# Performance work log

Measured on AMD Instinct MI355X. Metric: run time of the kernel, lower is better.

Reference implementation:

```python
import jax, jax.numpy as jnp
import numpy as np

TEMPERATURE = 0.07
DELTA = 0.3
KA = 2.0
R = 3
B = 4096
D = 512
K = 4096
N = 131072
N_DICT_KEYS = 3  # len(cluster_result) dict: inst2cluster/centroids/density


def _l2norm(x):
    # torch F.normalize: x / max(||x||, 1e-12)
    return x / jnp.maximum(jnp.linalg.norm(x, axis=-1, keepdims=True), 1e-12)


def _inst_inst(anchor, pos):
    # CE with label 0 on [diag, off-diag] == logsumexp(full row) - diag
    a = _l2norm(anchor)
    p = _l2norm(pos)
    logits = (a @ p.T) / TEMPERATURE  # [B, B]
    return jax.nn.logsumexp(logits, axis=1) - jnp.diagonal(logits)


def _off_diag_idx(b):
    # row i -> column indices [0..b-1] excluding i (row-major boolean-mask order)
    j = jnp.arange(b - 1)[None, :]
    return j + (j >= jnp.arange(b)[:, None]).astype(jnp.int32)


def _inst_proto(anchor, i2c, centroids, density, index):
    b = anchor.shape[0]
    a = _l2norm(anchor)
    oidx = _off_diag_idx(b)
    loss = jnp.zeros(b, dtype=anchor.dtype)
    for r in range(R):
        protos = _l2norm(centroids[r])           # [K, D]
        pid = i2c[r][index]                       # [B]
        sim = a @ protos[pid].T                   # [B, B]
        diag = jnp.diagonal(sim)
        off = jnp.take_along_axis(sim, oidx, axis=1)  # [B, B-1]
        # faithful to original: divide concatenated logits column-wise by density[pid]
        logits = jnp.concatenate([diag[:, None], off], axis=1) / density[r][pid][None, :]
        loss = loss + (jax.nn.logsumexp(logits, axis=1) - logits[:, 0])
        loss = loss / N_DICT_KEYS  # original divides INSIDE the loop
    return loss


def _weights(audio, frame, a_i2c, a_cent, f_i2c, f_cent, index):
    fa = _l2norm(audio)
    ff = _l2norm(frame)
    rho = jnp.sum(fa * ff, axis=1)  # diagonal of fa @ ff.T
    for r in range(R):
        ca = a_cent[r][a_i2c[r][index]]  # [B, D] (NOT normalized, as in original)
        cf = f_cent[r][f_i2c[r][index]]
        rho = rho - jnp.sum(ca * cf, axis=1)  # diagonal of ca @ cf.T
    order = jnp.argsort(rho)
    sorted_rho = rho[order]
    mu = rho.mean() + DELTA * rho.std()
    sigma = rho.std() * jnp.sqrt(jnp.asarray(KA, rho.dtype))
    y = jnp.exp(-0.5 * ((sorted_rho - mu) / sigma) ** 2) / (jnp.sqrt(2.0 * jnp.pi) * sigma)
    y = jnp.cumsum(y)
    y = y / y[-1]
    w = y[jnp.argsort(order)]  # y at the rank of each rho_i
    return jax.lax.stop_gradient(w)  # original detaches via cpu().numpy()


def _forward(audio_emb, frame_emb, a_centroids, a_density, f_centroids, f_density,
             video_index, a_inst2cluster, f_inst2cluster):
    loss_v2f_ii = _inst_inst(audio_emb, frame_emb)
    loss_f2v_ii = _inst_inst(frame_emb, audio_emb)
    loss_v2f_ip = _inst_proto(audio_emb, f_inst2cluster, f_centroids, f_density, video_index)
    loss_f2v_ip = _inst_proto(frame_emb, a_inst2cluster, a_centroids, a_density, video_index)
    w = _weights(audio_emb, frame_emb, a_inst2cluster, a_centroids,
                 f_inst2cluster, f_centroids, video_index)
    loss_v2f = jnp.sum(w * (loss_v2f_ii + loss_v2f_ip)) / jnp.sum(w)
    loss_f2v = jnp.sum(w * (loss_f2v_ii + loss_f2v_ip)) / jnp.sum(w)
    return loss_v2f + loss_f2v


def setup_inputs() -> dict:
    key = jax.random.key(0)
    ks = jax.random.split(key, 9)
    return {
        "audio_emb": jax.random.normal(ks[0], (B, D), jnp.float32),
        "frame_emb": jax.random.normal(ks[1], (B, D), jnp.float32),
        "a_centroids": jax.random.normal(ks[2], (R, K, D), jnp.float32),
        "a_density": jax.random.uniform(ks[3], (R, K), jnp.float32, 0.3, 1.3),
        "f_centroids": jax.random.normal(ks[4], (R, K, D), jnp.float32),
        "f_density": jax.random.uniform(ks[5], (R, K), jnp.float32, 0.3, 1.3),
        "video_index": jax.random.randint(ks[6], (B,), 0, N),
        "a_inst2cluster": jax.random.randint(ks[7], (R, N), 0, K),
        "f_inst2cluster": jax.random.randint(ks[8], (R, N), 0, K),
    }


def reference(audio_emb, frame_emb, a_centroids, a_density, f_centroids, f_density,
              video_index, a_inst2cluster, f_inst2cluster):
    return _forward(audio_emb, frame_emb, a_centroids, a_density, f_centroids, f_density,
                    video_index, a_inst2cluster, f_inst2cluster)
```

## Files before the change

### kernel.cpp

```cpp
#include <hip/hip_runtime.h>
#include <math.h>

#define B 4096
#define D 512
#define KC 4096
#define NIDX 131072
#define RR 3
#define TEMP 0.07f
#define M_II 14.5f
#define M_IP 4.0f

typedef __bf16 bf16x8 __attribute__((ext_vector_type(8)));
typedef float f32x4 __attribute__((ext_vector_type(4)));

__device__ __forceinline__ void gload_lds16(const void* g, void* l) {
  __builtin_amdgcn_global_load_lds(
      (const __attribute__((address_space(1))) unsigned int*)g,
      (__attribute__((address_space(3))) unsigned int*)l, 16, 0, 0);
}

__device__ __forceinline__ float dot8(float4 a0, float4 a1, float4 b0, float4 b1) {
  return a0.x * b0.x + a0.y * b0.y + a0.z * b0.z + a0.w * b0.w
       + a1.x * b1.x + a1.y * b1.y + a1.z * b1.z + a1.w * b1.w;
}

__global__ __launch_bounds__(256) void prep_kernel(
    const float* __restrict__ audio, const float* __restrict__ frame,
    const float* __restrict__ a_cent, const float* __restrict__ a_dens,
    const float* __restrict__ f_cent, const float* __restrict__ f_dens,
    const int* __restrict__ vidx, const int* __restrict__ a_i2c,
    const int* __restrict__ f_i2c,
    __bf16* __restrict__ Xa, __bf16* __restrict__ Xf,
    __bf16* __restrict__ Yf, __bf16* __restrict__ Ya,
    float* __restrict__ invdd_f, float* __restrict__ invdd_a,
    float* __restrict__ rho0, float* __restrict__ pcp) {
  const int u = blockIdx.x * 4 + (threadIdx.x >> 6);
  const int lane = threadIdx.x & 63;

  if (u < 2 * B) {
    const float* src; __bf16* dst;
    if (u < B) { src = audio + (size_t)u * D; dst = Xa + (size_t)u * D; }
    else       { src = frame + (size_t)(u - B) * D; dst = Xf + (size_t)(u - B) * D; }
    const float4* s4 = (const float4*)src + lane * 2;
    float4 v0 = s4[0], v1 = s4[1];
    float ss = dot8(v0, v1, v0, v1);
    #pragma unroll
    for (int off = 32; off >= 1; off >>= 1) ss += __shfl_xor(ss, off, 64);
    float invn = 1.f / fmaxf(sqrtf(ss), 1e-12f);
    __bf16 o[8];
    o[0] = (__bf16)(v0.x * invn); o[1] = (__bf16)(v0.y * invn);
    o[2] = (__bf16)(v0.z * invn); o[3] = (__bf16)(v0.w * invn);
    o[4] = (__bf16)(v1.x * invn); o[5] = (__bf16)(v1.y * invn);
    o[6] = (__bf16)(v1.z * invn); o[7] = (__bf16)(v1.w * invn);
    *(bf16x8*)(dst + lane * 8) = *(bf16x8*)o;
  } else if (u < 5 * B) {
    const int q = u - 2 * B;
    const int r = q >> 12;
    const int j = q & (B - 1);
    const int idx = vidx[j];
    const int fp = f_i2c[r * NIDX + idx];
    const int ap = a_i2c[r * NIDX + idx];
    const float4* fr4 = (const float4*)(f_cent + ((size_t)r * KC + fp) * D) + lane * 2;
    const float4* ar4 = (const float4*)(a_cent + ((size_t)r * KC + ap) * D) + lane * 2;
    float4 f0 = fr4[0], f1 = fr4[1];
    float4 a0 = ar4[0], a1 = ar4[1];
    float sf = dot8(f0, f1, f0, f1);
    float sa = dot8(a0, a1, a0, a1);
    float pc = dot8(a0, a1, f0, f1);
    #pragma unroll
    for (int off = 32; off >= 1; off >>= 1) {
      sf += __shfl_xor(sf, off, 64);
      sa += __shfl_xor(sa, off, 64);
      pc += __shfl_xor(pc, off, 64);
    }
    float invnf = 1.f / fmaxf(sqrtf(sf), 1e-12f);
    float invna = 1.f / fmaxf(sqrtf(sa), 1e-12f);
    const int slot = r * B + j;
    __bf16 of[8], oa[8];
    of[0] = (__bf16)(f0.x * invnf); of[1] = (__bf16)(f0.y * invnf);
    of[2] = (__bf16)(f0.z * invnf); of[3] = (__bf16)(f0.w * invnf);
    of[4] = (__bf16)(f1.x * invnf); of[5] = (__bf16)(f1.y * invnf);
    of[6] = (__bf16)(f1.z * invnf); of[7] = (__bf16)(f1.w * invnf);
    oa[0] = (__bf16)(a0.x * invna); oa[1] = (__bf16)(a0.y * invna);
    oa[2] = (__bf16)(a0.z * invna); oa[3] = (__bf16)(a0.w * invna);
    oa[4] = (__bf16)(a1.x * invna); oa[5] = (__bf16)(a1.y * invna);
    oa[6] = (__bf16)(a1.z * invna); oa[7] = (__bf16)(a1.w * invna);
    *(bf16x8*)(Yf + (size_t)slot * D + lane * 8) = *(bf16x8*)of;
    *(bf16x8*)(Ya + (size_t)slot * D + lane * 8) = *(bf16x8*)oa;
    if (lane == 0) {
      invdd_f[slot] = 1.f / f_dens[(size_t)r * KC + fp];
      invdd_a[slot] = 1.f / a_dens[(size_t)r * KC + ap];
      pcp[slot] = pc;
    }
  } else {
    const int i = u - 5 * B;
    const float4* x4 = (const float4*)(audio + (size_t)i * D) + lane * 2;
    const float4* y4 = (const float4*)(frame + (size_t)i * D) + lane * 2;
    float4 a0 = x4[0], a1 = x4[1], f0 = y4[0], f1 = y4[1];
    float saf = dot8(a0, a1, f0, f1);
    float sa = dot8(a0, a1, a0, a1);
    float sf = dot8(f0, f1, f0, f1);
    #pragma unroll
    for (int off = 32; off >= 1; off >>= 1) {
      saf += __shfl_xor(saf, off, 64);
      sa  += __shfl_xor(sa, off, 64);
      sf  += __shfl_xor(sf, off, 64);
    }
    if (lane == 0)
      rho0[i] = saf / (fmaxf(sqrtf(sa), 1e-12f) * fmaxf(sqrtf(sf), 1e-12f));
  }
}

__global__ __launch_bounds__(256) void lse_mfma_kernel(
    const __bf16* __restrict__ Xa, const __bf16* __restrict__ Xf,
    const __bf16* __restrict__ Yf, const __bf16* __restrict__ Ya,
    const float* __restrict__ invdd_f, const float* __restrict__ invdd_a,
    float* __restrict__ sp, float* __restrict__ colsp,
    float* __restrict__ diagAll) {
  __shared__ __bf16 As[128 * 32];
  __shared__ __bf16 Bs[128 * 32];
  __shared__ float inv_lds[2][132];
  __shared__ float part_s[2 * 128];
  __shared__ float colpart[2][128];

  const int yy = blockIdx.y;
  const int job = (yy == 0) ? 0 : yy + 1;
  const int hf = blockIdx.z;
  const int i0 = blockIdx.x * 128;

  const __bf16* Ab; const __bf16* Bb; const float* invArr = nullptr;
  if (job == 0)      { Ab = Xa; Bb = Xf; }
  else if (job <= 4) { Ab = Xa; Bb = Yf + (size_t)(job - 2) * B * D;
                       invArr = invdd_f + (job - 2) * B; }
  else               { Ab = Xf; Bb = Ya + (size_t)(job - 5) * B * D;
                       invArr = invdd_a + (job - 5) * B; }
  const bool ii = (job == 0);
  const float invT = 1.f / TEMP;
  const float inv0 = ii ? invT : invArr[0];
  const float MJ = ii ? M_II : M_IP;

  const int tid = threadIdx.x;
  const int wv = tid >> 6;
  const int lane = tid & 63;
  const int wr = (wv >> 1) * 64;
  const int wc = (wv & 1) * 64;
  const int g = lane >> 4;
  const int cl = lane & 15;

  const int srow = lane >> 2;
  const int skoff = (((lane & 3) ^ ((lane >> 3) & 3)) * 16);
  const int c0row = wv * 16 + srow;
  const int c1row = 64 + wv * 16 + srow;
  const char* gA0 = (const char*)Ab + (size_t)(i0 + c0row) * (D * 2) + skoff;
  const char* gA1 = (const char*)Ab + (size_t)(i0 + c1row) * (D * 2) + skoff;
  __bf16* lA0 = As + wv * 512;
  __bf16* lA1 = As + 2048 + wv * 512;
  __bf16* lB0 = Bs + wv * 512;
  __bf16* lB1 = Bs + 2048 + wv * 512;

  const int csw = (g ^ ((cl >> 1) & 3)) * 8;
  int aoff[4], boff[4];
  #pragma unroll
  for (int t = 0; t < 4; ++t) {
    aoff[t] = (wr + t * 16 + cl) * 32 + csw;
    boff[t] = (wc + t * 16 + cl) * 32 + csw;
  }

  float sacc[4][4];
  #pragma unroll
  for (int ri = 0; ri < 4; ++ri)
    #pragma unroll
    for (int v = 0; v < 4; ++v) sacc[ri][v] = 0.f;

  for (int jt = hf * 4; jt < hf * 4 + 4; ++jt) {
    const int j0 = jt * 128;
    float* invL = inv_lds[jt & 1];
    if (!ii && tid < 130) {
      int idx = j0 + tid; if (idx > B - 1) idx = B - 1;
      invL[tid] = invArr[idx];
    }
    const char* gB0 = (const char*)Bb + (size_t)(j0 + c0row) * (D * 2) + skoff;
    const char* gB1 = (const char*)Bb + (size_t)(j0 + c1row) * (D * 2) + skoff;

    f32x4 acc[4][4];
    #pragma unroll
    for (int ri = 0; ri < 4; ++ri)
      #pragma unroll
      for (int ci = 0; ci < 4; ++ci) acc[ri][ci] = (f32x4){0.f, 0.f, 0.f, 0.f};

    for (int kt = 0; kt < 16; ++kt) {
      __syncthreads();
      const int kb = kt * 64;
      gload_lds16(gA0 + kb, lA0);
      gload_lds16(gA1 + kb, lA1);
      gload_lds16(gB0 + kb, lB0);
      gload_lds16(gB1 + kb, lB1);
      __syncthreads();
      bf16x8 af[4], bfr[4];
      #pragma unroll
      for (int t = 0; t < 4; ++t) {
        af[t] = *(const bf16x8*)(As + aoff[t]);
        bfr[t] = *(const bf16x8*)(Bs + boff[t]);
      }
      #pragma unroll
      for (int ri = 0; ri < 4; ++ri)
        #pragma unroll
        for (int ci = 0; ci < 4; ++ci)
          acc[ri][ci] = __builtin_amdgcn_mfma_f32_16x16x32_bf16(
              af[ri], bfr[ci], acc[ri][ci], 0, 0, 0);
    }

    float csum[4] = {0.f, 0.f, 0.f, 0.f};
    #pragma unroll
    for (int ri = 0; ri < 4; ++ri) {
      #pragma unroll
      for (int v = 0; v < 4; ++v) {
        const int gi = i0 + wr + ri * 16 + g * 4 + v;
        float acc4 = 0.f;
        #pragma unroll
        for (int ci = 0; ci < 4; ++ci) {
          const int jloc = wc + ci * 16 + cl;
          const int gj = j0 + jloc;
          float sc;
          if (ii) sc = invT;
          else    sc = (gj == gi) ? inv0 : invL[(gj < gi) ? (jloc + 1) : jloc];
          float lv = acc[ri][ci][v] * sc;
          if (gj == gi) diagAll[(size_t)job * B + gi] = lv;
          float ev = __expf(lv - MJ);
          acc4 += ev;
          if (ii) csum[ci] += ev;
        }
        sacc[ri][v] += acc4;
      }
    }
    if (ii) {
      #pragma unroll
      for (int ci = 0; ci < 4; ++ci) {
        csum[ci] += __shfl_xor(csum[ci], 16, 64);
        csum[ci] += __shfl_xor(csum[ci], 32, 64);
      }
      if (g == 0) {
        #pragma unroll
        for (int ci = 0; ci < 4; ++ci)
          colpart[wv >> 1][wc + ci * 16 + cl] = csum[ci];
      }
      __syncthreads();
      if (tid < 128)
        colsp[(size_t)blockIdx.x * B + j0 + tid] =
            colpart[0][tid] + colpart[1][tid];
    }
  }

  #pragma unroll
  for (int ri = 0; ri < 4; ++ri) {
    #pragma unroll
    for (int v = 0; v < 4; ++v) {
      float s = sacc[ri][v];
      #pragma unroll
      for (int off = 8; off >= 1; off >>= 1) s += __shfl_xor(s, off, 64);
      if (cl == 0) part_s[(wv & 1) * 128 + wr + ri * 16 + g * 4 + v] = s;
    }
  }
  __syncthreads();
  if (tid < 128) {
    size_t o = ((size_t)job * 8 + hf) * B + i0 + tid;
    sp[o] = part_s[tid] + part_s[128 + tid];
  }
}

__global__ __launch_bounds__(256) void merge_rank_kernel(
    const float* __restrict__ sp, const float* __restrict__ colsp,
    const float* __restrict__ diagAll, const float* __restrict__ rho0,
    const float* __restrict__ pcp,
    float* __restrict__ lossAll, int* __restrict__ rankArr,
    float* __restrict__ srho) {
  __shared__ float lr[B];
  __shared__ float cnt[256];
  const int blk = blockIdx.x;
  const int t = threadIdx.x;
  if (blk < 128) {
    int idx = blk * 256 + t;
    int job = idx >> 12;
    int i = idx & (B - 1);
    if (job == 1) {
      float stot = 0.f;
      #pragma unroll 8
      for (int x = 0; x < 32; ++x) stot += colsp[(size_t)x * B + i];
      lossAll[idx] = M_II + logf(stot) - diagAll[i];
    } else {
      const float* s8 = sp + (size_t)job * 8 * B + i;
      float stot = 0.f;
      #pragma unroll
      for (int x = 0; x < 8; ++x) stot += s8[(size_t)x * B];
      float MJ = (job < 2) ? M_II : M_IP;
      lossAll[idx] = MJ + logf(stot) - diagAll[(size_t)job * B + i];
    }
  } else {
    const int base = (blk - 128) * 32;
    const int il = t & 31;
    const int i = base + il;
    const int jlo = (t >> 5) * 512;
    for (int k = t; k < B; k += 256)
      lr[k] = rho0[k] - pcp[k] - pcp[B + k] - pcp[2 * B + k];
    __syncthreads();
    float my = lr[i];
    int rk = 0;
    #pragma unroll 8
    for (int j = jlo; j < jlo + 512; ++j) {
      float v = lr[j];
      rk += (v < my) || (v == my && j < i);
    }
    cnt[t] = (float)rk;
    __syncthreads();
    if (t < 32) {
      int r = 0;
      #pragma unroll
      for (int s = 0; s < 8; ++s) r += (int)cnt[s * 32 + t];
      rankArr[i] = r;
      srho[r] = my;
    }
  }
}

__global__ __launch_bounds__(1024) void cdf_final_kernel(
    const float* __restrict__ srho, const int* __restrict__ rankArr,
    const float* __restrict__ lossAll, float* __restrict__ out) {
  __shared__ float pdf[B];
  __shared__ float wred[16], wr1[16], wr2[16];
  __shared__ float wexc[16];
  __shared__ float mv[3];
  const int t = threadIdx.x;
  const int lane = t & 63;
  const int wid = t >> 6;

  float4 sv = *reinterpret_cast<const float4*>(srho + (size_t)t * 4);
  float s = sv.x + sv.y + sv.z + sv.w;
  #pragma unroll
  for (int off = 32; off >= 1; off >>= 1) s += __shfl_xor(s, off, 64);
  if (lane == 0) wred[wid] = s;
  __syncthreads();
  if (t == 0) {
    float tot = 0.f;
    #pragma unroll
    for (int w = 0; w < 16; ++w) tot += wred[w];
    mv[0] = tot / (float)B;
  }
  __syncthreads();
  const float mean = mv[0];
  __syncthreads();
  float dx = sv.x - mean, dy = sv.y - mean, dz = sv.z - mean, dw = sv.w - mean;
  float v = dx * dx + dy * dy + dz * dz + dw * dw;
  #pragma unroll
  for (int off = 32; off >= 1; off >>= 1) v += __shfl_xor(v, off, 64);
  if (lane == 0) wred[wid] = v;
  __syncthreads();
  if (t == 0) {
    float tot = 0.f;
    #pragma unroll
    for (int w = 0; w < 16; ++w) tot += wred[w];
    float sd = sqrtf(tot / (float)B);
    mv[0] = mean + 0.3f * sd;
    mv[1] = sd * 1.41421356237f;
  }
  __syncthreads();
  const float mu = mv[0], sg = mv[1];
  const float c = 1.f / (2.5066282746310002f * sg);
  float p[4];
  {
    float z0 = (sv.x - mu) / sg; p[0] = expf(-0.5f * z0 * z0) * c;
    float z1 = (sv.y - mu) / sg; p[1] = expf(-0.5f * z1 * z1) * c;
    float z2 = (sv.z - mu) / sg; p[2] = expf(-0.5f * z2 * z2) * c;
    float z3 = (sv.w - mu) / sg; p[3] = expf(-0.5f * z3 * z3) * c;
  }
  float chunk = p[0] + p[1] + p[2] + p[3];
  float incl = chunk;
  #pragma unroll
  for (int d = 1; d < 64; d <<= 1) {
    float n = __shfl_up(incl, d, 64);
    if (lane >= d) incl += n;
  }
  if (lane == 63) wred[wid] = incl;
  __syncthreads();
  if (t == 0) {
    float run = 0.f;
    #pragma unroll
    for (int w = 0; w < 16; ++w) { wexc[w] = run; run += wred[w]; }
    mv[2] = run;
  }
  __syncthreads();
  float run = wexc[wid] + (incl - chunk);
  #pragma unroll
  for (int e = 0; e < 4; ++e) { run += p[e]; pdf[t * 4 + e] = run; }
  const float ylast = mv[2];
  __syncthreads();
  int4 rks = *reinterpret_cast<const int4*>(rankArr + (size_t)t * 4);
  float sw = 0.f, s1 = 0.f, s2 = 0.f;
  #pragma unroll
  for (int e = 0; e < 4; ++e) {
    const int i = t * 4 + e;
    const int rk = (e == 0) ? rks.x : (e == 1) ? rks.y : (e == 2) ? rks.z : rks.w;
    float wi = pdf[rk] / ylast;
    float lpv = lossAll[2 * B + i] * (1.f / 27.f) + lossAll[3 * B + i] * (1.f / 9.f)
              + lossAll[4 * B + i] * (1.f / 3.f);
    float lpf = lossAll[5 * B + i] * (1.f / 27.f) + lossAll[6 * B + i] * (1.f / 9.f)
              + lossAll[7 * B + i] * (1.f / 3.f);
    sw += wi;
    s1 += wi * (lossAll[i] + lpv);
    s2 += wi * (lossAll[B + i] + lpf);
  }
  #pragma unroll
  for (int off = 32; off >= 1; off >>= 1) {
    sw += __shfl_xor(sw, off, 64);
    s1 += __shfl_xor(s1, off, 64);
    s2 += __shfl_xor(s2, off, 64);
  }
  if (lane == 0) { wred[wid] = sw; wr1[wid] = s1; wr2[wid] = s2; }
  __syncthreads();
  if (t == 0) {
    float tw = 0.f, t1 = 0.f, t2 = 0.f;
    #pragma unroll
    for (int w = 0; w < 16; ++w) { tw += wred[w]; t1 += wr1[w]; t2 += wr2[w]; }
    out[0] = t1 / tw + t2 / tw;
  }
}

extern "C" void kernel_launch(void* const* d_in, const int* in_sizes, int n_in,
                              void* d_out, int out_size, void* d_ws, size_t ws_size,
                              hipStream_t stream) {
  const float* audio  = (const float*)d_in[0];
  const float* frame  = (const float*)d_in[1];
  const float* a_cent = (const float*)d_in[2];
  const float* a_dens = (const float*)d_in[3];
  const float* f_cent = (const float*)d_in[4];
  const float* f_dens = (const float*)d_in[5];
  const int* vidx  = (const int*)d_in[6];
  const int* a_i2c = (const int*)d_in[7];
  const int* f_i2c = (const int*)d_in[8];
  float* out = (float*)d_out;

  const size_t BD = (size_t)B * D;
  char* base = (char*)d_ws;
  __bf16* Xa = (__bf16*)base;              base += BD * 2;
  __bf16* Xf = (__bf16*)base;              base += BD * 2;
  __bf16* Yf = (__bf16*)base;              base += 3 * BD * 2;
  __bf16* Ya = (__bf16*)base;              base += 3 * BD * 2;
  float* invdd_f = (float*)base;           base += 3 * B * 4;
  float* invdd_a = (float*)base;           base += 3 * B * 4;
  float* rho0    = (float*)base;           base += B * 4;
  float* pcp     = (float*)base;           base += 3 * B * 4;
  float* sp      = (float*)base;           base += 64 * B * 4;
  float* colsp   = (float*)base;           base += 32 * B * 4;
  float* diagAll = (float*)base;           base += 8 * B * 4;
  float* lossAll = (float*)base;           base += 8 * B * 4;
  float* srho    = (float*)base;           base += B * 4;
  int*   rankArr = (int*)base;

  prep_kernel<<<(6 * B) / 4, 256, 0, stream>>>(audio, frame, a_cent, a_dens,
                                               f_cent, f_dens, vidx, a_i2c, f_i2c,
                                               Xa, Xf, Yf, Ya, invdd_f, invdd_a,
                                               rho0, pcp);

  dim3 g2(B / 128, 7, 8);
  lse_mfma_kernel<<<g2, 256, 0, stream>>>(Xa, Xf, Yf, Ya, invdd_f, invdd_a,
                                          sp, colsp, diagAll);

  merge_rank_kernel<<<256, 256, 0, stream>>>(sp, colsp, diagAll, rho0, pcp,
                                             lossAll, rankArr, srho);
  cdf_final_kernel<<<1, 1024, 0, stream>>>(srho, rankArr, lossAll, out);
}
```

Baseline: 345.5 us.

## Enlarge LSE GEMM tile to 256x256 with 512 threads, one tile per block

The fused similarity/logsumexp MFMA kernel now computes one 256x256 output tile per 512-thread block, where before each 256-thread block looped over four 128x128 column tiles. Each wave holds an 8x4 grid of 16x16 accumulators, so each staged k-slice is reused across more MFMAs. The per-column density scale lookup is simplified to a fixed offset on off-diagonal tiles. This is meant to cut global/LDS traffic per FLOP and per-tile loop overhead. In exchange it raises register pressure (128 accumulator floats per lane plus sacc), which may reduce occupancy, and it doubles the partial-sum buffer read by the merge kernel.

New measurement: 348.2 us. Within noise of the previous version (+0.8%).

```diff
diff --git a/kernel.cpp b/kernel.cpp
--- a/kernel.cpp
+++ b/kernel.cpp
@@ -111,22 +111,22 @@
   }
 }
 
-__global__ __launch_bounds__(256) void lse_mfma_kernel(
+__global__ __launch_bounds__(512) void lse_mfma_kernel(
     const __bf16* __restrict__ Xa, const __bf16* __restrict__ Xf,
     const __bf16* __restrict__ Yf, const __bf16* __restrict__ Ya,
     const float* __restrict__ invdd_f, const float* __restrict__ invdd_a,
     float* __restrict__ sp, float* __restrict__ colsp,
     float* __restrict__ diagAll) {
-  __shared__ __bf16 As[128 * 32];
-  __shared__ __bf16 Bs[128 * 32];
-  __shared__ float inv_lds[2][132];
-  __shared__ float part_s[2 * 128];
-  __shared__ float colpart[2][128];
+  __shared__ __bf16 As[256 * 32];
+  __shared__ __bf16 Bs[256 * 32];
+  __shared__ float invL[260];
+  __shared__ float part_s[4 * 256];
+  __shared__ float colpart[2][256];
 
   const int yy = blockIdx.y;
   const int job = (yy == 0) ? 0 : yy + 1;
-  const int hf = blockIdx.z;
-  const int i0 = blockIdx.x * 128;
+  const int i0 = blockIdx.x * 256;
+  const int j0 = blockIdx.z * 256;
 
   const __bf16* Ab; const __bf16* Bb; const float* invArr = nullptr;
   if (job == 0)      { Ab = Xa; Bb = Xf; }
@@ -142,129 +142,120 @@
   const int tid = threadIdx.x;
   const int wv = tid >> 6;
   const int lane = tid & 63;
-  const int wr = (wv >> 1) * 64;
-  const int wc = (wv & 1) * 64;
+  const int wr = (wv >> 2) * 128;
+  const int wc = (wv & 3) * 64;
   const int g = lane >> 4;
   const int cl = lane & 15;
+
+  if (!ii && tid < 258) {
+    int idx = j0 + tid; if (idx > B - 1) idx = B - 1;
+    invL[tid] = invArr[idx];
+  }
 
   const int srow = lane >> 2;
   const int skoff = (((lane & 3) ^ ((lane >> 3) & 3)) * 16);
   const int c0row = wv * 16 + srow;
-  const int c1row = 64 + wv * 16 + srow;
   const char* gA0 = (const char*)Ab + (size_t)(i0 + c0row) * (D * 2) + skoff;
-  const char* gA1 = (const char*)Ab + (size_t)(i0 + c1row) * (D * 2) + skoff;
+  const char* gA1 = gA0 + (size_t)128 * (D * 2);
+  const char* gB0 = (const char*)Bb + (size_t)(j0 + c0row) * (D * 2) + skoff;
+  const char* gB1 = gB0 + (size_t)128 * (D * 2);
   __bf16* lA0 = As + wv * 512;
-  __bf16* lA1 = As + 2048 + wv * 512;
+  __bf16* lA1 = As + 4096 + wv * 512;
   __bf16* lB0 = Bs + wv * 512;
-  __bf16* lB1 = Bs + 2048 + wv * 512;
+  __bf16* lB1 = Bs + 4096 + wv * 512;
 
   const int csw = (g ^ ((cl >> 1) & 3)) * 8;
-  int aoff[4], boff[4];
-  #pragma unroll
-  for (int t = 0; t < 4; ++t) {
-    aoff[t] = (wr + t * 16 + cl) * 32 + csw;
-    boff[t] = (wc + t * 16 + cl) * 32 + csw;
-  }
-
-  float sacc[4][4];
-  #pragma unroll
-  for (int ri = 0; ri < 4; ++ri)
-    #pragma unroll
-    for (int v = 0; v < 4; ++v) sacc[ri][v] = 0.f;
-
-  for (int jt = hf * 4; jt < hf * 4 + 4; ++jt) {
-    const int j0 = jt * 128;
-    float* invL = inv_lds[jt & 1];
-    if (!ii && tid < 130) {
-      int idx = j0 + tid; if (idx > B - 1) idx = B - 1;
-      invL[tid] = invArr[idx];
-    }
-    const char* gB0 = (const char*)Bb + (size_t)(j0 + c0row) * (D * 2) + skoff;
-    const char* gB1 = (const char*)Bb + (size_t)(j0 + c1row) * (D * 2) + skoff;
-
-    f32x4 acc[4][4];
-    #pragma unroll
-    for (int ri = 0; ri < 4; ++ri)
-      #pragma unroll
-      for (int ci = 0; ci < 4; ++ci) acc[ri][ci] = (f32x4){0.f, 0.f, 0.f, 0.f};
-
-    for (int kt = 0; kt < 16; ++kt) {
-      __syncthreads();
-      const int kb = kt * 64;
-      gload_lds16(gA0 + kb, lA0);
-      gload_lds16(gA1 + kb, lA1);
-      gload_lds16(gB0 + kb, lB0);
-      gload_lds16(gB1 + kb, lB1);
-      __syncthreads();
-      bf16x8 af[4], bfr[4];
-      #pragma unroll
-      for (int t = 0; t < 4; ++t) {
-        af[t] = *(const bf16x8*)(As + aoff[t]);
-        bfr[t] = *(const bf16x8*)(Bs + boff[t]);
+  int aoff[8], boff[4];
+  #pragma unroll
+  for (int t = 0; t < 8; ++t) aoff[t] = (wr + t * 16 + cl) * 32 + csw;
+  #pragma unroll
+  for (int t = 0; t < 4; ++t) boff[t] = (wc + t * 16 + cl) * 32 + csw;
+
+  f32x4 acc[8][4];
+  #pragma unroll
+  for (int ri = 0; ri < 8; ++ri)
+    #pragma unroll
+    for (int ci = 0; ci < 4; ++ci) acc[ri][ci] = (f32x4){0.f, 0.f, 0.f, 0.f};
+
+  for (int kt = 0; kt < 16; ++kt) {
+    __syncthreads();
+    const int kb = kt * 64;
+    gload_lds16(gA0 + kb, lA0);
+    gload_lds16(gA1 + kb, lA1);
+    gload_lds16(gB0 + kb, lB0);
+    gload_lds16(gB1 + kb, lB1);
+    __syncthreads();
+    bf16x8 af[8], bfr[4];
+    #pragma unroll
+    for (int t = 0; t < 8; ++t) af[t] = *(const bf16x8*)(As + aoff[t]);
+    #pragma unroll
+    for (int t = 0; t < 4; ++t) bfr[t] = *(const bf16x8*)(Bs + boff[t]);
+    #pragma unroll
+    for (int ri = 0; ri < 8; ++ri)
+      #pragma unroll
+      for (int ci = 0; ci < 4; ++ci)
+        acc[ri][ci] = __builtin_amdgcn_mfma_f32_16x16x32_bf16(
+            af[ri], bfr[ci], acc[ri][ci], 0, 0, 0);
+  }
+
+  const bool dtile = (blockIdx.x == blockIdx.z);
+  const int co = (j0 < i0) ? 1 : 0;
+  float sacc[8][4];
+  float csum[4] = {0.f, 0.f, 0.f, 0.f};
+  #pragma unroll
+  for (int ri = 0; ri < 8; ++ri) {
+    #pragma unroll
+    for (int v = 0; v < 4; ++v) {
+      const int gi = i0 + wr + ri * 16 + g * 4 + v;
+      float acc4 = 0.f;
+      #pragma unroll
+      for (int ci = 0; ci < 4; ++ci) {
+        const int jloc = wc + ci * 16 + cl;
+        const int gj = j0 + jloc;
+        float sc;
+        if (ii) sc = invT;
+        else if (!dtile) sc = invL[jloc + co];
+        else sc = (gj == gi) ? inv0 : invL[(gj < gi) ? (jloc + 1) : jloc];
+        float lv = acc[ri][ci][v] * sc;
+        if (dtile && gj == gi) diagAll[(size_t)job * B + gi] = lv;
+        float ev = __expf(lv - MJ);
+        acc4 += ev;
+        if (ii) csum[ci] += ev;
       }
-      #pragma unroll
-      for (int ri = 0; ri < 4; ++ri)
-        #pragma unroll
-        for (int ci = 0; ci < 4; ++ci)
-          acc[ri][ci] = __builtin_amdgcn_mfma_f32_16x16x32_bf16(
-              af[ri], bfr[ci], acc[ri][ci], 0, 0, 0);
-    }
-
-    float csum[4] = {0.f, 0.f, 0.f, 0.f};
-    #pragma unroll
-    for (int ri = 0; ri < 4; ++ri) {
-      #pragma unroll
-      for (int v = 0; v < 4; ++v) {
-        const int gi = i0 + wr + ri * 16 + g * 4 + v;
-        float acc4 = 0.f;
-        #pragma unroll
-        for (int ci = 0; ci < 4; ++ci) {
-          const int jloc = wc + ci * 16 + cl;
-          const int gj = j0 + jloc;
-          float sc;
-          if (ii) sc = invT;
-          else    sc = (gj == gi) ? inv0 : invL[(gj < gi) ? (jloc + 1) : jloc];
-          float lv = acc[ri][ci][v] * sc;
-          if (gj == gi) diagAll[(size_t)job * B + gi] = lv;
-          float ev = __expf(lv - MJ);
-          acc4 += ev;
-          if (ii) csum[ci] += ev;
-        }
-        sacc[ri][v] += acc4;
-      }
-    }
-    if (ii) {
-      #pragma unroll
-      for (int ci = 0; ci < 4; ++ci) {
-        csum[ci] += __shfl_xor(csum[ci], 16, 64);
-        csum[ci] += __shfl_xor(csum[ci], 32, 64);
-      }
-      if (g == 0) {
-        #pragma unroll
-        for (int ci = 0; ci < 4; ++ci)
-          colpart[wv >> 1][wc + ci * 16 + cl] = csum[ci];
-      }
-      __syncthreads();
-      if (tid < 128)
-        colsp[(size_t)blockIdx.x * B + j0 + tid] =
-            colpart[0][tid] + colpart[1][tid];
-    }
-  }
-
-  #pragma unroll
-  for (int ri = 0; ri < 4; ++ri) {
+      sacc[ri][v] = acc4;
+    }
+  }
+  if (ii) {
+    #pragma unroll
+    for (int ci = 0; ci < 4; ++ci) {
+      csum[ci] += __shfl_xor(csum[ci], 16, 64);
+      csum[ci] += __shfl_xor(csum[ci], 32, 64);
+    }
+    if (g == 0) {
+      #pragma unroll
+      for (int ci = 0; ci < 4; ++ci)
+        colpart[wv >> 2][wc + ci * 16 + cl] = csum[ci];
+    }
+    __syncthreads();
+    if (tid < 256)
+      colsp[(size_t)blockIdx.x * B + j0 + tid] =
+          colpart[0][tid] + colpart[1][tid];
+  }
+
+  #pragma unroll
+  for (int ri = 0; ri < 8; ++ri) {
     #pragma unroll
     for (int v = 0; v < 4; ++v) {
       float s = sacc[ri][v];
       #pragma unroll
       for (int off = 8; off >= 1; off >>= 1) s += __shfl_xor(s, off, 64);
-      if (cl == 0) part_s[(wv & 1) * 128 + wr + ri * 16 + g * 4 + v] = s;
-    }
-  }
-  __syncthreads();
-  if (tid < 128) {
-    size_t o = ((size_t)job * 8 + hf) * B + i0 + tid;
-    sp[o] = part_s[tid] + part_s[128 + tid];
+      if (cl == 0) part_s[(wv & 3) * 256 + wr + ri * 16 + g * 4 + v] = s;
+    }
+  }
+  __syncthreads();
+  if (tid < 256) {
+    size_t o = ((size_t)job * 16 + blockIdx.z) * B + i0 + tid;
+    sp[o] = part_s[tid] + part_s[256 + tid] + part_s[512 + tid] + part_s[768 + tid];
   }
 }
 
@@ -284,14 +275,14 @@
     int i = idx & (B - 1);
     if (job == 1) {
       float stot = 0.f;
-      #pragma unroll 8
-      for (int x = 0; x < 32; ++x) stot += colsp[(size_t)x * B + i];
+      #pragma unroll
+      for (int x = 0; x < 16; ++x) stot += colsp[(size_t)x * B + i];
       lossAll[idx] = M_II + logf(stot) - diagAll[i];
     } else {
-      const float* s8 = sp + (size_t)job * 8 * B + i;
+      const float* s16 = sp + (size_t)job * 16 * B + i;
       float stot = 0.f;
       #pragma unroll
-      for (int x = 0; x < 8; ++x) stot += s8[(size_t)x * B];
+      for (int x = 0; x < 16; ++x) stot += s16[(size_t)x * B];
       float MJ = (job < 2) ? M_II : M_IP;
       lossAll[idx] = MJ + logf(stot) - diagAll[(size_t)job * B + i];
     }
@@ -448,8 +439,8 @@
   float* invdd_a = (float*)base;           base += 3 * B * 4;
   float* rho0    = (float*)base;           base += B * 4;
   float* pcp     = (float*)base;           base += 3 * B * 4;
-  float* sp      = (float*)base;           base += 64 * B * 4;
-  float* colsp   = (float*)base;           base += 32 * B * 4;
+  float* sp      = (float*)base;           base += 128 * B * 4;
+  float* colsp   = (float*)base;           base += 16 * B * 4;
   float* diagAll = (float*)base;           base += 8 * B * 4;
   float* lossAll = (float*)base;           base += 8 * B * 4;
   float* srho    = (float*)base;           base += B * 4;
@@ -460,8 +451,8 @@
                                                Xa, Xf, Yf, Ya, invdd_f, invdd_a,
                                                rho0, pcp);
 
-  dim3 g2(B / 128, 7, 8);
-  lse_mfma_kernel<<<g2, 256, 0, stream>>>(Xa, Xf, Yf, Ya, invdd_f, invdd_a,
+  dim3 g2(16, 7, 16);
+  lse_mfma_kernel<<<g2, 512, 0, stream>>>(Xa, Xf, Yf, Ya, invdd_f, invdd_a,
                                           sp, colsp, diagAll);
 
   merge_rank_kernel<<<256, 256, 0, stream>>>(sp, colsp, diagAll, rho0, pcp,
```
